# Optimization experiments

Measured on AMD Instinct MI355X. Metric: run time of the kernel, lower is better.

Reference implementation:

```python
import jax, jax.numpy as jnp
import numpy as np

B, S, H, DH = 2, 2048, 16, 64
D = H * DH


def setup_inputs() -> dict:
    key = jax.random.key(0)
    ks = jax.random.split(key, 10)
    std = 0.02
    return {
        "hidden_states": jax.random.normal(ks[0], (B, S, D), jnp.float32),
        "mask": jax.random.randint(ks[1], (B, S), 0, 2, jnp.int64 if jax.config.jax_enable_x64 else jnp.int32),
        "Wq": jax.random.normal(ks[2], (D, D), jnp.float32) * std,
        "bq": jnp.zeros((D,), jnp.float32),
        "Wk": jax.random.normal(ks[3], (D, D), jnp.float32) * std,
        "bk": jnp.zeros((D,), jnp.float32),
        "Wv": jax.random.normal(ks[4], (D, D), jnp.float32) * std,
        "bv": jnp.zeros((D,), jnp.float32),
        "Wo": jax.random.normal(ks[5], (D, D), jnp.float32) * std,
        "bo": jnp.zeros((D,), jnp.float32),
    }


def _split_heads(x):
    # (B, S, H*DH) -> (B, H, S, DH)
    b, s, _ = x.shape
    return x.reshape(b, s, H, DH).transpose(0, 2, 1, 3)


def reference(hidden_states, mask, Wq, bq, Wk, bk, Wv, bv, Wo, bo):
    # Linear projections (torch nn.Linear: x @ W.T + b)
    q = _split_heads(hidden_states @ Wq.T + bq)
    k = _split_heads(hidden_states @ Wk.T + bk)
    v = _split_heads(hidden_states @ Wv.T + bv)

    scale = 1.0 / np.sqrt(DH).astype(np.float32)
    scores = jnp.einsum("bhqd,bhkd->bhqk", q, k) * scale  # (B,H,S,S)
    # mask out padded key positions (mask==0 -> -inf), broadcast over heads/queries
    scores = jnp.where(mask[:, None, None, :] == 0, -jnp.inf, scores)
    weights = jax.nn.softmax(scores, axis=-1)

    attended = jnp.einsum("bhqk,bhkd->bhqd", weights, v)  # (B,H,S,DH)
    merged = attended.transpose(0, 2, 1, 3).reshape(hidden_states.shape)  # (B,S,D)
    return merged @ Wo.T + bo
```

## Files before the change

kernel.cpp:

```cpp
#include <hip/hip_runtime.h>
#include <hip/hip_bf16.h>

typedef __bf16 bf16;
typedef __bf16 bf16x4 __attribute__((ext_vector_type(4)));
typedef __bf16 bf16x8 __attribute__((ext_vector_type(8)));
typedef float f32x4 __attribute__((ext_vector_type(4)));

#define B_ 2
#define S_ 2048
#define H_ 16
#define DH_ 64
#define D_ 1024
#define NT_ 4096

#define WAIT_VMCNT0() asm volatile("s_waitcnt vmcnt(0)" ::: "memory")
#define WAIT_LGKM0()  asm volatile("s_waitcnt lgkmcnt(0)" ::: "memory")

__device__ __forceinline__ void gld_lds16(const bf16* g, bf16* l) {
    __builtin_amdgcn_global_load_lds(
        (__attribute__((address_space(1))) void*)g,
        (__attribute__((address_space(3))) void*)l, 16, 0, 0);
}

__device__ __forceinline__ bf16 f2bf(float x) {
    union { float f; unsigned u; } v; v.f = x;
    unsigned short h = (unsigned short)((v.u + 0x7FFF + ((v.u >> 16) & 1)) >> 16);
    return __builtin_bit_cast(bf16, h);
}

__global__ __launch_bounds__(256) void cvt_kernel(
    const float* __restrict__ hs,
    const float* __restrict__ Wq, const float* __restrict__ Wk,
    const float* __restrict__ Wv, const float* __restrict__ Wo,
    bf16* __restrict__ hsb, bf16* __restrict__ wqkv, bf16* __restrict__ wob)
{
    int i = (blockIdx.x * 256 + threadIdx.x) * 4;
    const float* src;
    bf16* dst;
    if (i < 4194304) {
        src = hs + i; dst = hsb + i;
    } else if (i < 7340032) {
        int off = i - 4194304;
        int which = off >> 20;
        int within = off & 1048575;
        src = (which == 0 ? Wq : which == 1 ? Wk : Wv) + within;
        dst = wqkv + off;
    } else {
        int off = i - 7340032;
        src = Wo + off; dst = wob + off;
    }
    float4 v = *(const float4*)src;
    bf16x4 o = { (bf16)v.x, (bf16)v.y, (bf16)v.z, (bf16)v.w };
    *(bf16x4*)dst = o;
}

__global__ __launch_bounds__(256, 2) void gemm_bt(
    const bf16* __restrict__ A, const bf16* __restrict__ Bm,
    int mode,
    const float* __restrict__ b0, const float* __restrict__ b1,
    const float* __restrict__ b2,
    bf16* __restrict__ Qo, bf16* __restrict__ Ko, bf16* __restrict__ Vt,
    float* __restrict__ Co)
{
    const int K = 1024;
    __shared__ __attribute__((aligned(16))) bf16 sA[128 * 32];
    __shared__ __attribute__((aligned(16))) bf16 sB[128 * 32];

    int tid = threadIdx.x;
    int wave = tid >> 6, lane = tid & 63;
    int quad = lane >> 4, l16 = lane & 15;
    int m0 = blockIdx.x * 128;
    int n0 = blockIdx.y * 128;
    int wm = (wave & 1) * 64, wn = (wave >> 1) * 64;
    int fs = (l16 >> 1) & 3;

    f32x4 acc[4][4];
#pragma unroll
    for (int i = 0; i < 4; i++)
#pragma unroll
        for (int j = 0; j < 4; j++) acc[i][j] = (f32x4){0.f, 0.f, 0.f, 0.f};

    for (int k0 = 0; k0 < K; k0 += 32) {
#pragma unroll
        for (int i = 0; i < 2; i++) {
            int chunk = tid + i * 256;
            int row = chunk >> 2;
            int kc = ((chunk & 3) ^ ((row >> 1) & 3)) * 8;
            gld_lds16(A + (size_t)(m0 + row) * K + k0 + kc, &sA[chunk * 8]);
            gld_lds16(Bm + (size_t)(n0 + row) * K + k0 + kc, &sB[chunk * 8]);
        }
        WAIT_VMCNT0();
        __syncthreads();

        bf16x8 af[4], bfr[4];
#pragma unroll
        for (int i = 0; i < 4; i++)
            af[i] = *(const bf16x8*)&sA[(wm + i * 16 + l16) * 32 + (quad ^ fs) * 8];
#pragma unroll
        for (int j = 0; j < 4; j++)
            bfr[j] = *(const bf16x8*)&sB[(wn + j * 16 + l16) * 32 + (quad ^ fs) * 8];
#pragma unroll
        for (int i = 0; i < 4; i++)
#pragma unroll
            for (int j = 0; j < 4; j++)
                acc[i][j] = __builtin_amdgcn_mfma_f32_16x16x32_bf16(
                    af[i], bfr[j], acc[i][j], 0, 0, 0);
        __syncthreads();
    }

    if (mode == 0) {
        const float QSCALE = 0.125f * 1.44269504088896340736f;
#pragma unroll
        for (int j = 0; j < 4; j++) {
            int n = n0 + wn + j * 16 + l16;
            int region = n >> 10;
            int nn = n & 1023;
            int h = nn >> 6, d = nn & 63;
            float bias = (region == 0 ? b0 : region == 1 ? b1 : b2)[nn];
#pragma unroll
            for (int i = 0; i < 4; i++)
#pragma unroll
                for (int r = 0; r < 4; r++) {
                    int m = m0 + wm + i * 16 + quad * 4 + r;
                    int b = m >> 11, s = m & 2047;
                    int bh = b * H_ + h;
                    float v = acc[i][j][r] + bias;
                    if (region == 0)
                        Qo[((size_t)bh * S_ + s) * DH_ + d] = f2bf(v * QSCALE);
                    else if (region == 1)
                        Ko[((size_t)bh * S_ + s) * DH_ + d] = f2bf(v);
                    else
                        Vt[((size_t)bh * DH_ + d) * S_ + s] = f2bf(v);
                }
        }
    } else {
#pragma unroll
        for (int j = 0; j < 4; j++) {
            int n = n0 + wn + j * 16 + l16;
            float bias = b0[n];
#pragma unroll
            for (int i = 0; i < 4; i++)
#pragma unroll
                for (int r = 0; r < 4; r++) {
                    int m = m0 + wm + i * 16 + quad * 4 + r;
                    Co[(size_t)m * D_ + n] = acc[i][j][r] + bias;
                }
        }
    }
}

__global__ __launch_bounds__(256, 4) void attn_kernel(
    const bf16* __restrict__ Q, const bf16* __restrict__ Kg,
    const bf16* __restrict__ Vt, const int* __restrict__ mask,
    bf16* __restrict__ Og)
{
    __shared__ __attribute__((aligned(16))) bf16 sK[64 * 64];
    __shared__ __attribute__((aligned(16))) bf16 sV[64 * 64];
    __shared__ __attribute__((aligned(16))) bf16 sP[4][16 * 64];
    __shared__ float sMaddAll[S_];

    int tid = threadIdx.x;
    int wave = tid >> 6, lane = tid & 63;
    int quad = lane >> 4, l16 = lane & 15;
    int bh = blockIdx.y;
    int b = bh >> 4;
    int q0 = blockIdx.x * 64;
    int f8 = l16 & 7;

    const bf16* Qb = Q + (size_t)bh * S_ * DH_;
    const bf16* Kb = Kg + (size_t)bh * S_ * DH_;
    const bf16* Vb = Vt + (size_t)bh * DH_ * S_;

#pragma unroll
    for (int i = 0; i < S_ / 256; i++) {
        int idx = tid + i * 256;
        sMaddAll[idx] = mask[b * S_ + idx] ? 0.f : -1e30f;
    }

    int qrow = q0 + wave * 16 + l16;
    bf16x8 aq0 = *(const bf16x8*)&Qb[(size_t)qrow * DH_ + quad * 8];
    bf16x8 aq1 = *(const bf16x8*)&Qb[(size_t)qrow * DH_ + 32 + quad * 8];

    f32x4 o[4];
#pragma unroll
    for (int i = 0; i < 4; i++) o[i] = (f32x4){0.f, 0.f, 0.f, 0.f};
    float psum[4] = {0.f, 0.f, 0.f, 0.f};

    __syncthreads();

    for (int kt = 0; kt < S_; kt += 64) {
#pragma unroll
        for (int i = 0; i < 2; i++) {
            int chunk = tid + i * 256;
            int row = chunk >> 3;
            int cc = ((chunk & 7) ^ (row & 7)) * 8;
            gld_lds16(&Kb[(size_t)(kt + row) * DH_ + cc], &sK[chunk * 8]);
            gld_lds16(&Vb[(size_t)row * S_ + kt + cc], &sV[chunk * 8]);
        }
        WAIT_VMCNT0();
        __syncthreads();

#pragma unroll
        for (int nt = 0; nt < 4; nt++) {
            bf16x8 bk0 = *(const bf16x8*)&sK[(nt * 16 + l16) * 64 + (quad ^ f8) * 8];
            bf16x8 bk1 = *(const bf16x8*)&sK[(nt * 16 + l16) * 64 + ((quad + 4) ^ f8) * 8];
            f32x4 c = (f32x4){0.f, 0.f, 0.f, 0.f};
            c = __builtin_amdgcn_mfma_f32_16x16x32_bf16(aq0, bk0, c, 0, 0, 0);
            c = __builtin_amdgcn_mfma_f32_16x16x32_bf16(aq1, bk1, c, 0, 0, 0);
            float ma = sMaddAll[kt + nt * 16 + l16];
#pragma unroll
            for (int r = 0; r < 4; r++) {
                float p = __builtin_amdgcn_exp2f(c[r] + ma);
                psum[r] += p;
                int row = quad * 4 + r;
                int g = (nt * 2 + (l16 >> 3)) ^ (row & 7);
                sP[wave][row * 64 + g * 8 + (l16 & 7)] = f2bf(p);
            }
        }

        WAIT_LGKM0();
        bf16x8 ap0 = *(const bf16x8*)&sP[wave][l16 * 64 + (quad ^ f8) * 8];
        bf16x8 ap1 = *(const bf16x8*)&sP[wave][l16 * 64 + ((quad + 4) ^ f8) * 8];
#pragma unroll
        for (int dt = 0; dt < 4; dt++) {
            bf16x8 bv0 = *(const bf16x8*)&sV[(dt * 16 + l16) * 64 + (quad ^ f8) * 8];
            bf16x8 bv1 = *(const bf16x8*)&sV[(dt * 16 + l16) * 64 + ((quad + 4) ^ f8) * 8];
            o[dt] = __builtin_amdgcn_mfma_f32_16x16x32_bf16(ap0, bv0, o[dt], 0, 0, 0);
            o[dt] = __builtin_amdgcn_mfma_f32_16x16x32_bf16(ap1, bv1, o[dt], 0, 0, 0);
        }
        __syncthreads();
    }

    int h = bh & 15;
#pragma unroll
    for (int r = 0; r < 4; r++) {
        float v = psum[r];
        v += __shfl_xor(v, 1);
        v += __shfl_xor(v, 2);
        v += __shfl_xor(v, 4);
        v += __shfl_xor(v, 8);
        float rcp = 1.f / v;
        int s = q0 + wave * 16 + quad * 4 + r;
#pragma unroll
        for (int dt = 0; dt < 4; dt++) {
            int d = dt * 16 + l16;
            Og[((size_t)(b * S_ + s)) * D_ + h * 64 + d] = f2bf(o[dt][r] * rcp);
        }
    }
}

extern "C" void kernel_launch(void* const* d_in, const int* in_sizes, int n_in,
                              void* d_out, int out_size, void* d_ws, size_t ws_size,
                              hipStream_t stream) {
    const float* hs = (const float*)d_in[0];
    const int* mask = (const int*)d_in[1];
    const float* Wq = (const float*)d_in[2];
    const float* bq = (const float*)d_in[3];
    const float* Wk = (const float*)d_in[4];
    const float* bk = (const float*)d_in[5];
    const float* Wv = (const float*)d_in[6];
    const float* bv = (const float*)d_in[7];
    const float* Wo = (const float*)d_in[8];
    const float* bo = (const float*)d_in[9];
    float* out = (float*)d_out;

    char* ws = (char*)d_ws;
    bf16* hsb  = (bf16*)(ws);
    bf16* wqkv = (bf16*)(ws + ((size_t)8 << 20));
    bf16* wob  = (bf16*)(ws + ((size_t)14 << 20));
    bf16* Qw   = (bf16*)(ws + ((size_t)16 << 20));
    bf16* Kw   = (bf16*)(ws + ((size_t)24 << 20));
    bf16* Vtw  = (bf16*)(ws + ((size_t)32 << 20));
    bf16* attn = (bf16*)(ws + ((size_t)40 << 20));

    cvt_kernel<<<8192, 256, 0, stream>>>(hs, Wq, Wk, Wv, Wo, hsb, wqkv, wob);
    gemm_bt<<<dim3(32, 24), 256, 0, stream>>>(hsb, wqkv, 0, bq, bk, bv,
                                              Qw, Kw, Vtw, nullptr);
    attn_kernel<<<dim3(32, 32), 256, 0, stream>>>(Qw, Kw, Vtw, mask, attn);
    gemm_bt<<<dim3(32, 8), 256, 0, stream>>>(attn, wob, 1, bo, nullptr, nullptr,
                                             nullptr, nullptr, nullptr, out);
}
```

Baseline: 213.8 us.

## Double-buffer LDS tiles in GEMM and attention kernels to overlap loads

Both the projection GEMM and the attention kernel now use two LDS buffers. The next K (or K/V) tile is issued with global_load_lds right after the barrier, while MFMA runs on the current tile, and the trailing barrier is dropped. This is meant to hide global memory latency behind compute. The cost is twice the LDS footprint, with attention launch bounds lowered from 4 to 3 blocks per CU to fit. The per-wave sP buffer is now reused across iterations without a trailing barrier, which relies on the leading barrier for ordering.

```diff
diff --git a/kernel.cpp b/kernel.cpp
--- a/kernel.cpp
+++ b/kernel.cpp
@@ -63,8 +63,9 @@
     float* __restrict__ Co)
 {
     const int K = 1024;
-    __shared__ __attribute__((aligned(16))) bf16 sA[128 * 32];
-    __shared__ __attribute__((aligned(16))) bf16 sB[128 * 32];
+    const int NIT = K / 32;
+    __shared__ __attribute__((aligned(16))) bf16 sA[2][128 * 32];
+    __shared__ __attribute__((aligned(16))) bf16 sB[2][128 * 32];
 
     int tid = threadIdx.x;
     int wave = tid >> 6, lane = tid & 63;
@@ -74,38 +75,49 @@
     int wm = (wave & 1) * 64, wn = (wave >> 1) * 64;
     int fs = (l16 >> 1) & 3;
 
+    int chunk0 = tid, chunk1 = tid + 256;
+    int row0 = chunk0 >> 2, row1 = chunk1 >> 2;
+    int kc0 = ((chunk0 & 3) ^ ((row0 >> 1) & 3)) * 8;
+    int kc1 = ((chunk1 & 3) ^ ((row1 >> 1) & 3)) * 8;
+
     f32x4 acc[4][4];
 #pragma unroll
     for (int i = 0; i < 4; i++)
 #pragma unroll
         for (int j = 0; j < 4; j++) acc[i][j] = (f32x4){0.f, 0.f, 0.f, 0.f};
 
-    for (int k0 = 0; k0 < K; k0 += 32) {
-#pragma unroll
-        for (int i = 0; i < 2; i++) {
-            int chunk = tid + i * 256;
-            int row = chunk >> 2;
-            int kc = ((chunk & 3) ^ ((row >> 1) & 3)) * 8;
-            gld_lds16(A + (size_t)(m0 + row) * K + k0 + kc, &sA[chunk * 8]);
-            gld_lds16(Bm + (size_t)(n0 + row) * K + k0 + kc, &sB[chunk * 8]);
-        }
+    gld_lds16(A + (size_t)(m0 + row0) * K + 0 + kc0, &sA[0][chunk0 * 8]);
+    gld_lds16(Bm + (size_t)(n0 + row0) * K + 0 + kc0, &sB[0][chunk0 * 8]);
+    gld_lds16(A + (size_t)(m0 + row1) * K + 0 + kc1, &sA[0][chunk1 * 8]);
+    gld_lds16(Bm + (size_t)(n0 + row1) * K + 0 + kc1, &sB[0][chunk1 * 8]);
+
+    for (int it = 0; it < NIT; it++) {
+        int cur = it & 1;
         WAIT_VMCNT0();
         __syncthreads();
 
+        if (it + 1 < NIT) {
+            int k0 = (it + 1) * 32;
+            int nxt = cur ^ 1;
+            gld_lds16(A + (size_t)(m0 + row0) * K + k0 + kc0, &sA[nxt][chunk0 * 8]);
+            gld_lds16(Bm + (size_t)(n0 + row0) * K + k0 + kc0, &sB[nxt][chunk0 * 8]);
+            gld_lds16(A + (size_t)(m0 + row1) * K + k0 + kc1, &sA[nxt][chunk1 * 8]);
+            gld_lds16(Bm + (size_t)(n0 + row1) * K + k0 + kc1, &sB[nxt][chunk1 * 8]);
+        }
+
         bf16x8 af[4], bfr[4];
 #pragma unroll
         for (int i = 0; i < 4; i++)
-            af[i] = *(const bf16x8*)&sA[(wm + i * 16 + l16) * 32 + (quad ^ fs) * 8];
+            af[i] = *(const bf16x8*)&sA[cur][(wm + i * 16 + l16) * 32 + (quad ^ fs) * 8];
 #pragma unroll
         for (int j = 0; j < 4; j++)
-            bfr[j] = *(const bf16x8*)&sB[(wn + j * 16 + l16) * 32 + (quad ^ fs) * 8];
+            bfr[j] = *(const bf16x8*)&sB[cur][(wn + j * 16 + l16) * 32 + (quad ^ fs) * 8];
 #pragma unroll
         for (int i = 0; i < 4; i++)
 #pragma unroll
             for (int j = 0; j < 4; j++)
                 acc[i][j] = __builtin_amdgcn_mfma_f32_16x16x32_bf16(
                     af[i], bfr[j], acc[i][j], 0, 0, 0);
-        __syncthreads();
     }
 
     if (mode == 0) {
@@ -149,13 +161,13 @@
     }
 }
 
-__global__ __launch_bounds__(256, 4) void attn_kernel(
+__global__ __launch_bounds__(256, 3) void attn_kernel(
     const bf16* __restrict__ Q, const bf16* __restrict__ Kg,
     const bf16* __restrict__ Vt, const int* __restrict__ mask,
     bf16* __restrict__ Og)
 {
-    __shared__ __attribute__((aligned(16))) bf16 sK[64 * 64];
-    __shared__ __attribute__((aligned(16))) bf16 sV[64 * 64];
+    __shared__ __attribute__((aligned(16))) bf16 sK[2][64 * 64];
+    __shared__ __attribute__((aligned(16))) bf16 sV[2][64 * 64];
     __shared__ __attribute__((aligned(16))) bf16 sP[4][16 * 64];
     __shared__ float sMaddAll[S_];
 
@@ -177,6 +189,11 @@
         sMaddAll[idx] = mask[b * S_ + idx] ? 0.f : -1e30f;
     }
 
+    int chunk0 = tid, chunk1 = tid + 256;
+    int krow0 = chunk0 >> 3, krow1 = chunk1 >> 3;
+    int cc0 = ((chunk0 & 7) ^ (krow0 & 7)) * 8;
+    int cc1 = ((chunk1 & 7) ^ (krow1 & 7)) * 8;
+
     int qrow = q0 + wave * 16 + l16;
     bf16x8 aq0 = *(const bf16x8*)&Qb[(size_t)qrow * DH_ + quad * 8];
     bf16x8 aq1 = *(const bf16x8*)&Qb[(size_t)qrow * DH_ + 32 + quad * 8];
@@ -186,24 +203,31 @@
     for (int i = 0; i < 4; i++) o[i] = (f32x4){0.f, 0.f, 0.f, 0.f};
     float psum[4] = {0.f, 0.f, 0.f, 0.f};
 
-    __syncthreads();
-
-    for (int kt = 0; kt < S_; kt += 64) {
-#pragma unroll
-        for (int i = 0; i < 2; i++) {
-            int chunk = tid + i * 256;
-            int row = chunk >> 3;
-            int cc = ((chunk & 7) ^ (row & 7)) * 8;
-            gld_lds16(&Kb[(size_t)(kt + row) * DH_ + cc], &sK[chunk * 8]);
-            gld_lds16(&Vb[(size_t)row * S_ + kt + cc], &sV[chunk * 8]);
-        }
+    gld_lds16(&Kb[(size_t)krow0 * DH_ + cc0], &sK[0][chunk0 * 8]);
+    gld_lds16(&Vb[(size_t)krow0 * S_ + 0 + cc0], &sV[0][chunk0 * 8]);
+    gld_lds16(&Kb[(size_t)krow1 * DH_ + cc1], &sK[0][chunk1 * 8]);
+    gld_lds16(&Vb[(size_t)krow1 * S_ + 0 + cc1], &sV[0][chunk1 * 8]);
+
+    const int NIT = S_ / 64;
+    for (int it = 0; it < NIT; it++) {
+        int cur = it & 1;
+        int kt = it * 64;
         WAIT_VMCNT0();
         __syncthreads();
 
+        if (it + 1 < NIT) {
+            int ktn = kt + 64;
+            int nxt = cur ^ 1;
+            gld_lds16(&Kb[(size_t)(ktn + krow0) * DH_ + cc0], &sK[nxt][chunk0 * 8]);
+            gld_lds16(&Vb[(size_t)krow0 * S_ + ktn + cc0], &sV[nxt][chunk0 * 8]);
+            gld_lds16(&Kb[(size_t)(ktn + krow1) * DH_ + cc1], &sK[nxt][chunk1 * 8]);
+            gld_lds16(&Vb[(size_t)krow1 * S_ + ktn + cc1], &sV[nxt][chunk1 * 8]);
+        }
+
 #pragma unroll
         for (int nt = 0; nt < 4; nt++) {
-            bf16x8 bk0 = *(const bf16x8*)&sK[(nt * 16 + l16) * 64 + (quad ^ f8) * 8];
-            bf16x8 bk1 = *(const bf16x8*)&sK[(nt * 16 + l16) * 64 + ((quad + 4) ^ f8) * 8];
+            bf16x8 bk0 = *(const bf16x8*)&sK[cur][(nt * 16 + l16) * 64 + (quad ^ f8) * 8];
+            bf16x8 bk1 = *(const bf16x8*)&sK[cur][(nt * 16 + l16) * 64 + ((quad + 4) ^ f8) * 8];
             f32x4 c = (f32x4){0.f, 0.f, 0.f, 0.f};
             c = __builtin_amdgcn_mfma_f32_16x16x32_bf16(aq0, bk0, c, 0, 0, 0);
             c = __builtin_amdgcn_mfma_f32_16x16x32_bf16(aq1, bk1, c, 0, 0, 0);
@@ -223,12 +247,11 @@
         bf16x8 ap1 = *(const bf16x8*)&sP[wave][l16 * 64 + ((quad + 4) ^ f8) * 8];
 #pragma unroll
         for (int dt = 0; dt < 4; dt++) {
-            bf16x8 bv0 = *(const bf16x8*)&sV[(dt * 16 + l16) * 64 + (quad ^ f8) * 8];
-            bf16x8 bv1 = *(const bf16x8*)&sV[(dt * 16 + l16) * 64 + ((quad + 4) ^ f8) * 8];
+            bf16x8 bv0 = *(const bf16x8*)&sV[cur][(dt * 16 + l16) * 64 + (quad ^ f8) * 8];
+            bf16x8 bv1 = *(const bf16x8*)&sV[cur][(dt * 16 + l16) * 64 + ((quad + 4) ^ f8) * 8];
             o[dt] = __builtin_amdgcn_mfma_f32_16x16x32_bf16(ap0, bv0, o[dt], 0, 0, 0);
             o[dt] = __builtin_amdgcn_mfma_f32_16x16x32_bf16(ap1, bv1, o[dt], 0, 0, 0);
         }
-        __syncthreads();
     }
 
     int h = bh & 15;
```

Measured after the change: 229.0 us. +7.1%, slower.
